# Performance work log

Measured on AMD Instinct MI355X. Metric: run time of the kernel, lower is better.

## Reference

```python
import jax, jax.numpy as jnp
import numpy as np

NUM_EMBED = 512
EMBED_DIM = 64
COMMITMENT_COST = 0.25
DECAY = 0.99
LAPLACE_ALPHA = 1e-05


def setup_inputs() -> dict:
    key = jax.random.key(0)
    k1, k2 = jax.random.split(key, 2)
    inputs = jax.random.normal(k1, (4, EMBED_DIM, 32, 32, 32), dtype=jnp.float32)
    embed = jax.random.normal(k2, (NUM_EMBED, EMBED_DIM), dtype=jnp.float32)
    # buffers: embed_avg starts as a clone of embed; cluster_size at steady state (post first pass)
    embed_avg = embed
    cluster_size = jnp.ones((NUM_EMBED,), dtype=jnp.float32)
    return {"inputs": inputs, "embed": embed, "embed_avg": embed_avg, "cluster_size": cluster_size}


def reference(inputs, embed, embed_avg, cluster_size):
    # channel-last flatten: [B,C,D,H,W] -> [B,D,H,W,C] -> [N,C]
    channel_last = jnp.transpose(inputs, (0, 2, 3, 4, 1))
    input_shape = channel_last.shape
    flat_input = channel_last.reshape(-1, EMBED_DIM)  # [N, C]
    n_tokens = flat_input.shape[0]

    distances = ((flat_input ** 2).sum(axis=1, keepdims=True)
                 + (embed ** 2).sum(axis=1)
                 - 2.0 * flat_input @ embed.T)
    encoding_indices = jnp.argmin(distances, axis=1)  # [N]

    quantized_cl = embed[encoding_indices].reshape(input_shape)  # gather + reshape

    # --- EMA codebook update (training branch), all non-differentiable ---
    # new_cluster_size = one_hot.sum(0); dw = one_hot.T @ flat_input  (as segment sums)
    new_counts = jax.ops.segment_sum(jnp.ones((n_tokens,), flat_input.dtype),
                                     encoding_indices, num_segments=NUM_EMBED)
    dw = jax.ops.segment_sum(flat_input, encoding_indices, num_segments=NUM_EMBED)  # [K, C]
    new_cluster_size = cluster_size * DECAY + (1.0 - DECAY) * new_counts
    new_embed_avg = embed_avg * DECAY + (1.0 - DECAY) * dw
    n = new_cluster_size.sum()
    smoothed = n * ((new_cluster_size + LAPLACE_ALPHA) / (n + NUM_EMBED * LAPLACE_ALPHA))
    new_embed = new_embed_avg / smoothed[:, None]

    # perplexity from empirical code usage
    avg_probs = new_counts / n_tokens
    perplexity = jnp.exp(-jnp.sum(avg_probs * jnp.log(avg_probs + 1e-10)))

    quantized_cf = jnp.transpose(quantized_cl, (0, 4, 1, 2, 3))  # back to [B,C,D,H,W]

    # commitment loss (quantized is detached in original; everything above is no_grad)
    e_latent_loss = jnp.mean((quantized_cf - inputs) ** 2)
    loss = COMMITMENT_COST * e_latent_loss

    # straight-through estimator
    quantized_out = inputs + jax.lax.stop_gradient(quantized_cf - inputs)

    encoding_indices = encoding_indices.reshape(input_shape[:-1])
    return (loss, quantized_out, perplexity, encoding_indices,
            new_embed, new_cluster_size, new_embed_avg)
```

## Files before the change

### kernel.cpp

```cpp
#include <hip/hip_runtime.h>
#include <math.h>

typedef __attribute__((ext_vector_type(8))) short s16x8;
typedef __attribute__((ext_vector_type(4))) float f32x4;

#define B_    4
#define C_    64
#define S_    32768
#define N_    131072
#define K_    512
#define SPLITS 8
#define DECAY_ 0.99f
#define ONEM_  0.01f
#define ALPHA_ 1e-5f
#define DELTA_ 0.01f
#define AMB_CAP 65536

#define OFF_LOSS 0
#define OFF_Q    1
#define OFF_PERP 8388609
#define OFF_IDX  8388610
#define OFF_NEMB 8519682
#define OFF_NCS  8552450
#define OFF_NEA  8552962

#define WS_LOSS   0
#define WS_AMBN   8
#define WS_CNT    16
#define WS_CUR    528
#define WS_OFFS   1040
#define WS_SMOOTH 1552
#define WS_E2     2064
#define WS_SORT   2576
#define WS_PART   133648
#define WS_SPL    395792
#define WS_AMB    444944
#define WS_ET     510480

__device__ __forceinline__ ushort f2bf(float f) {
    uint u = __float_as_uint(f);
    u = u + 0x7FFFu + ((u >> 16) & 1u);
    return (ushort)(u >> 16);
}
__device__ __forceinline__ float bf2f(ushort h) {
    return __uint_as_float(((uint)h) << 16);
}

__global__ __launch_bounds__(256) void k_split(const float* __restrict__ embed,
                                               float* __restrict__ wsf) {
    const int t = threadIdx.x;
    const int lane = t & 63;
    const int code = blockIdx.x * 4 + (t >> 6);
    const float e = embed[code * C_ + lane];
    const float sc = -2.f * e;
    const ushort h1 = f2bf(sc);
    const ushort h2 = f2bf(sc - bf2f(h1));
    ushort* tab = (ushort*)(wsf + WS_SPL);
    tab[0 * (K_ * C_) + code * C_ + lane] = h1;
    tab[1 * (K_ * C_) + code * C_ + lane] = h2;
    wsf[WS_ET + lane * K_ + code] = e;
    float sq = e * e;
    for (int o = 32; o > 0; o >>= 1) sq += __shfl_down(sq, o, 64);
    if (lane == 0) wsf[WS_E2 + code] = sq;
}

__global__ __launch_bounds__(256) void k_assign(const float* __restrict__ in,
                                                float* __restrict__ out,
                                                float* __restrict__ wsf,
                                                int* __restrict__ wsi) {
    __shared__ float s_e2l[K_];
    __shared__ int   s_cnt[K_];
    __shared__ float s_x2[256];
    __shared__ float s_loss;

    const int t = threadIdx.x;
    const int lane = t & 63;
    const int w = t >> 6;
    const int col = lane & 15;
    const int quad = lane >> 4;

    for (int i = t; i < K_; i += 256) { s_e2l[i] = wsf[WS_E2 + i]; s_cnt[i] = 0; }
    if (t == 0) s_loss = 0.f;

    const int nw = blockIdx.x * 256 + w * 64;

    s16x8 a[4][2][2];
#pragma unroll
    for (int j = 0; j < 4; ++j) {
        const int n = nw + j * 16 + col;
        const int base = ((n >> 15) << 21) + (n & (S_ - 1));
        float x0[8], x1[8];
#pragma unroll
        for (int q = 0; q < 8; ++q) {
            x0[q] = in[base + ((quad * 8 + q) << 15)];
            x1[q] = in[base + ((32 + quad * 8 + q) << 15)];
        }
        float x2 = 0.f;
#pragma unroll
        for (int q = 0; q < 8; ++q) x2 += x0[q] * x0[q] + x1[q] * x1[q];
        x2 += __shfl_xor(x2, 16, 64);
        x2 += __shfl_xor(x2, 32, 64);
        if (quad == 0) s_x2[w * 64 + j * 16 + col] = x2;

        float4* q0 = (float4*)(out + OFF_Q + (size_t)n * C_ + quad * 8);
        q0[0] = make_float4(x0[0], x0[1], x0[2], x0[3]);
        q0[1] = make_float4(x0[4], x0[5], x0[6], x0[7]);
        float4* q1 = (float4*)(out + OFF_Q + (size_t)n * C_ + 32 + quad * 8);
        q1[0] = make_float4(x1[0], x1[1], x1[2], x1[3]);
        q1[1] = make_float4(x1[4], x1[5], x1[6], x1[7]);

#pragma unroll
        for (int q = 0; q < 8; ++q) {
            ushort h = f2bf(x0[q]); a[j][0][0][q] = (short)h;
            a[j][1][0][q] = (short)f2bf(x0[q] - bf2f(h));
            h = f2bf(x1[q]); a[j][0][1][q] = (short)h;
            a[j][1][1][q] = (short)f2bf(x1[q] - bf2f(h));
        }
    }
    __syncthreads();

    const s16x8* tab = (const s16x8*)(wsf + WS_SPL);
    float bestd[4][4], bestd2[4][4];
    int   besti[4][4];
#pragma unroll
    for (int j = 0; j < 4; ++j)
#pragma unroll
        for (int r = 0; r < 4; ++r) { bestd[j][r] = 3.4e38f; bestd2[j][r] = 3.4e38f; besti[j][r] = 0; }

    int o = col * 8 + quad;
    s16x8 bh0 = tab[o], bh1 = tab[o + 4];
    s16x8 bl0 = tab[4096 + o], bl1 = tab[4096 + o + 4];

    for (int ct = 0; ct < 32; ++ct) {
        s16x8 nh0, nh1, nl0, nl1;
        if (ct < 31) {
            const int on = o + 128;
            nh0 = tab[on];        nh1 = tab[on + 4];
            nl0 = tab[4096 + on]; nl1 = tab[4096 + on + 4];
        }
        const float e2c = s_e2l[ct * 16 + col];
        f32x4 acc[4];
#pragma unroll
        for (int j = 0; j < 4; ++j) acc[j] = (f32x4){e2c, e2c, e2c, e2c};
#pragma unroll
        for (int j = 0; j < 4; ++j) acc[j] = __builtin_amdgcn_mfma_f32_16x16x32_bf16(a[j][1][0], bh0, acc[j], 0, 0, 0);
#pragma unroll
        for (int j = 0; j < 4; ++j) acc[j] = __builtin_amdgcn_mfma_f32_16x16x32_bf16(a[j][1][1], bh1, acc[j], 0, 0, 0);
#pragma unroll
        for (int j = 0; j < 4; ++j) acc[j] = __builtin_amdgcn_mfma_f32_16x16x32_bf16(a[j][0][0], bl0, acc[j], 0, 0, 0);
#pragma unroll
        for (int j = 0; j < 4; ++j) acc[j] = __builtin_amdgcn_mfma_f32_16x16x32_bf16(a[j][0][1], bl1, acc[j], 0, 0, 0);
#pragma unroll
        for (int j = 0; j < 4; ++j) acc[j] = __builtin_amdgcn_mfma_f32_16x16x32_bf16(a[j][0][0], bh0, acc[j], 0, 0, 0);
#pragma unroll
        for (int j = 0; j < 4; ++j) acc[j] = __builtin_amdgcn_mfma_f32_16x16x32_bf16(a[j][0][1], bh1, acc[j], 0, 0, 0);

        const int code = ct * 16 + col;
#pragma unroll
        for (int j = 0; j < 4; ++j) {
#pragma unroll
            for (int r = 0; r < 4; ++r) {
                const float av = acc[j][r];
                bestd2[j][r] = fminf(bestd2[j][r], fmaxf(av, bestd[j][r]));
                if (av < bestd[j][r]) { bestd[j][r] = av; besti[j][r] = code; }
            }
        }
        bh0 = nh0; bh1 = nh1; bl0 = nl0; bl1 = nl1;
        o += 128;
    }

    float lsum = 0.f;
#pragma unroll
    for (int j = 0; j < 4; ++j) {
#pragma unroll
        for (int r = 0; r < 4; ++r) {
            float d1 = bestd[j][r], d2 = bestd2[j][r]; int i1 = besti[j][r];
            for (int m = 1; m <= 8; m <<= 1) {
                const float d1o = __shfl_xor(d1, m, 64);
                const int   i1o = __shfl_xor(i1, m, 64);
                const float d2o = __shfl_xor(d2, m, 64);
                if (d1o < d1 || (d1o == d1 && i1o < i1)) {
                    d2 = fminf(d1, d2o); d1 = d1o; i1 = i1o;
                } else {
                    d2 = fminf(d2, d1o);
                }
            }
            if (col == 0) {
                const int tok = j * 16 + quad * 4 + r;
                out[OFF_IDX + nw + tok] = (float)i1;
                atomicAdd(&s_cnt[i1], 1);
                lsum += d1 + s_x2[w * 64 + tok];
                if (d2 - d1 < DELTA_) {
                    const int pos = atomicAdd(&wsi[WS_AMBN], 1);
                    if (pos < AMB_CAP) wsi[WS_AMB + pos] = nw + tok;
                }
            }
        }
    }
    if (col == 0) atomicAdd(&s_loss, lsum);
    __syncthreads();
    for (int i = t; i < K_; i += 256) {
        const int v = s_cnt[i];
        if (v) atomicAdd(&wsi[WS_CNT + i], v);
    }
    if (t == 0) atomicAdd(&wsf[WS_LOSS], s_loss);
}

__global__ __launch_bounds__(256) void k_fixup(float* __restrict__ out,
                                               const float* __restrict__ wsf,
                                               int* __restrict__ wsi) {
    __shared__ float sx[4][C_];
    const int t = threadIdx.x;
    const int lane = t & 63;
    const int w = t >> 6;
    const int gw = blockIdx.x * 4 + w;
    const int nw = gridDim.x * 4;
    int cntA = wsi[WS_AMBN];
    if (cntA > AMB_CAP) cntA = AMB_CAP;
    const float* eT = wsf + WS_ET;

    for (int a = gw; a < cntA; a += nw) {
        const int n = wsi[WS_AMB + a];
        const float xv = out[OFF_Q + (size_t)n * C_ + lane];
        sx[w][lane] = xv;
        float x2 = xv * xv;
        for (int m = 1; m <= 32; m <<= 1) x2 += __shfl_xor(x2, m, 64);

        float bd = 3.4e38f; int bi = 0;
#pragma unroll 2
        for (int q = 0; q < 8; ++q) {
            const int k = (q << 6) + lane;
            float d0 = 0.f, d1 = 0.f, d2 = 0.f, d3 = 0.f;
#pragma unroll
            for (int c = 0; c < C_; c += 4) {
                d0 += sx[w][c + 0] * eT[(c + 0) * K_ + k];
                d1 += sx[w][c + 1] * eT[(c + 1) * K_ + k];
                d2 += sx[w][c + 2] * eT[(c + 2) * K_ + k];
                d3 += sx[w][c + 3] * eT[(c + 3) * K_ + k];
            }
            const float dist = x2 + wsf[WS_E2 + k] - 2.f * ((d0 + d1) + (d2 + d3));
            if (dist < bd) { bd = dist; bi = k; }
        }
        for (int m = 1; m <= 32; m <<= 1) {
            const float db = __shfl_xor(bd, m, 64);
            const int   ib = __shfl_xor(bi, m, 64);
            if (db < bd || (db == bd && ib < bi)) { bd = db; bi = ib; }
        }
        if (lane == 0) {
            const int old = (int)out[OFF_IDX + n];
            if (bi != old) {
                out[OFF_IDX + n] = (float)bi;
                atomicAdd(&wsi[WS_CNT + old], -1);
                atomicAdd(&wsi[WS_CNT + bi], 1);
            }
        }
    }
}

__global__ __launch_bounds__(512) void k_stats(const float* __restrict__ cs,
                                               float* __restrict__ out,
                                               float* __restrict__ wsf,
                                               int* __restrict__ wsi) {
    __shared__ float sf[K_];
    __shared__ int   si[K_];
    const int t = threadIdx.x;

    const int cnt = wsi[WS_CNT + t];
    const float ncs = cs[t] * DECAY_ + ONEM_ * (float)cnt;
    out[OFF_NCS + t] = ncs;

    sf[t] = ncs;
    __syncthreads();
    for (int o = 256; o > 0; o >>= 1) {
        if (t < o) sf[t] += sf[t + o];
        __syncthreads();
    }
    const float n = sf[0];
    __syncthreads();

    const float ap = (float)cnt / (float)N_;
    sf[t] = ap * logf(ap + 1e-10f);
    __syncthreads();
    for (int o = 256; o > 0; o >>= 1) {
        if (t < o) sf[t] += sf[t + o];
        __syncthreads();
    }
    if (t == 0) {
        out[OFF_PERP] = expf(-sf[0]);
        out[OFF_LOSS] = 0.25f * wsf[WS_LOSS] / (float)((long long)N_ * C_);
    }

    wsf[WS_SMOOTH + t] = n * (ncs + ALPHA_) / (n + (float)K_ * ALPHA_);

    si[t] = cnt;
    __syncthreads();
    for (int o = 1; o < K_; o <<= 1) {
        int v = (t >= o) ? si[t - o] : 0;
        __syncthreads();
        si[t] += v;
        __syncthreads();
    }
    wsi[WS_OFFS + t] = si[t] - cnt;
}

#define SCT 1024
__global__ __launch_bounds__(256) void k_scatter(const float* __restrict__ out,
                                                 int* __restrict__ wsi) {
    __shared__ int hc[K_];
    __shared__ int lc[K_];
    __shared__ int codes[SCT];
    const int t = threadIdx.x;
    const int base = blockIdx.x * SCT;

    for (int i = t; i < K_; i += 256) { hc[i] = 0; lc[i] = 0; }
    __syncthreads();
#pragma unroll
    for (int j = 0; j < SCT / 256; ++j) {
        const int k = (int)out[OFF_IDX + base + j * 256 + t];
        codes[j * 256 + t] = k;
        atomicAdd(&hc[k], 1);
    }
    __syncthreads();
    for (int i = t; i < K_; i += 256) {
        const int c = hc[i];
        int gbase = 0;
        if (c > 0) gbase = atomicAdd(&wsi[WS_CUR + i], c);
        hc[i] = wsi[WS_OFFS + i] + gbase;
    }
    __syncthreads();
#pragma unroll
    for (int j = 0; j < SCT / 256; ++j) {
        const int k = codes[j * 256 + t];
        const int pos = atomicAdd(&lc[k], 1);
        wsi[WS_SORT + hc[k] + pos] = base + j * 256 + t;
    }
}

__global__ __launch_bounds__(64) void k_dw_split(float* __restrict__ out,
                                                 float* __restrict__ wsf,
                                                 const int* __restrict__ wsi) {
    const int lane = threadIdx.x;
    const int k = blockIdx.x >> 3;
    const int p = blockIdx.x & (SPLITS - 1);
    const int off = wsi[WS_OFFS + k];
    const int cnt = wsi[WS_CNT + k];
    const int chunk = (cnt + SPLITS - 1) >> 3;
    const int j0 = p * chunk;
    const int j1 = min(j0 + chunk, cnt);
    const float* fx = out + OFF_Q;
    const int* sort = wsi + WS_SORT + off;

    float acc = 0.f;
    for (int base = j0; base < j1; base += 64) {
        const int mcnt = min(64, j1 - base);
        int id = 0;
        if (base + lane < j1) id = sort[base + lane];
        int m = 0;
        for (; m + 8 <= mcnt; m += 8) {
            const int t0 = __shfl(id, m + 0, 64);
            const int t1 = __shfl(id, m + 1, 64);
            const int t2 = __shfl(id, m + 2, 64);
            const int t3 = __shfl(id, m + 3, 64);
            const int t4 = __shfl(id, m + 4, 64);
            const int t5 = __shfl(id, m + 5, 64);
            const int t6 = __shfl(id, m + 6, 64);
            const int t7 = __shfl(id, m + 7, 64);
            const float v0 = fx[(size_t)t0 * C_ + lane];
            const float v1 = fx[(size_t)t1 * C_ + lane];
            const float v2 = fx[(size_t)t2 * C_ + lane];
            const float v3 = fx[(size_t)t3 * C_ + lane];
            const float v4 = fx[(size_t)t4 * C_ + lane];
            const float v5 = fx[(size_t)t5 * C_ + lane];
            const float v6 = fx[(size_t)t6 * C_ + lane];
            const float v7 = fx[(size_t)t7 * C_ + lane];
            acc += ((v0 + v1) + (v2 + v3)) + ((v4 + v5) + (v6 + v7));
        }
        for (; m < mcnt; ++m) {
            const int tk = __shfl(id, m, 64);
            acc += fx[(size_t)tk * C_ + lane];
        }
    }
    wsf[WS_PART + (size_t)blockIdx.x * C_ + lane] = acc;
}

__global__ __launch_bounds__(256) void k_ema(const float* __restrict__ embed_avg,
                                             float* __restrict__ out,
                                             const float* __restrict__ wsf) {
    const int i = blockIdx.x * 256 + threadIdx.x;
    const int k = i >> 6;
    const int c = i & 63;
    float dw = 0.f;
#pragma unroll
    for (int p = 0; p < SPLITS; ++p)
        dw += wsf[WS_PART + (size_t)(k * SPLITS + p) * C_ + c];
    const float nea = embed_avg[i] * DECAY_ + ONEM_ * dw;
    out[OFF_NEA + i] = nea;
    out[OFF_NEMB + i] = nea / wsf[WS_SMOOTH + k];
}

__global__ __launch_bounds__(256) void k_quant(const float* __restrict__ embed,
                                               float* __restrict__ out) {
    const int t = threadIdx.x;
    const int n = blockIdx.x * 256 + t;
    const int b = n >> 15;
    const int s = n & (S_ - 1);
    const int base = (b << 21) + s;
    const int k = (int)out[OFF_IDX + n];
    const float4* er = (const float4*)(embed + k * C_);
#pragma unroll
    for (int q = 0; q < 16; ++q) {
        float4 v = er[q];
        out[OFF_Q + base + ((4*q + 0) << 15)] = v.x;
        out[OFF_Q + base + ((4*q + 1) << 15)] = v.y;
        out[OFF_Q + base + ((4*q + 2) << 15)] = v.z;
        out[OFF_Q + base + ((4*q + 3) << 15)] = v.w;
    }
}

extern "C" void kernel_launch(void* const* d_in, const int* in_sizes, int n_in,
                              void* d_out, int out_size, void* d_ws, size_t ws_size,
                              hipStream_t stream) {
    const float* in        = (const float*)d_in[0];
    const float* embed     = (const float*)d_in[1];
    const float* embed_avg = (const float*)d_in[2];
    const float* cs        = (const float*)d_in[3];
    float* out = (float*)d_out;
    float* wsf = (float*)d_ws;
    int*   wsi = (int*)d_ws;

    hipMemsetAsync(d_ws, 0, (WS_CUR + K_) * sizeof(int), stream);

    k_split   <<<K_ / 4, 256, 0, stream>>>(embed, wsf);
    k_assign  <<<N_ / 256, 256, 0, stream>>>(in, out, wsf, wsi);
    k_fixup   <<<256, 256, 0, stream>>>(out, wsf, wsi);
    k_stats   <<<1, K_, 0, stream>>>(cs, out, wsf, wsi);
    k_scatter <<<N_ / SCT, 256, 0, stream>>>(out, wsi);
    k_dw_split<<<K_ * SPLITS, 64, 0, stream>>>(out, wsf, wsi);
    k_ema     <<<K_ * C_ / 256, 256, 0, stream>>>(embed_avg, out, wsf);
    k_quant   <<<N_ / 256, 256, 0, stream>>>(embed, out);
}
```

Before: 210.5 us.

## Split codebook search across wave pairs and merge partial argmins in LDS

Each block now handles 128 tokens instead of 256. Two waves share each 64-token group, and each wave scans half of the 512 codes. The per-half best and second-best distances and indices are written to shared memory and merged by the first wave before the index, count, loss and ambiguity bookkeeping. This doubles the grid and shortens the per-wave MFMA loop, which should give more parallelism and better latency hiding. In exchange both waves load the input and do the bf16 split redundantly, and an extra barrier and LDS merge are added.

```diff
diff --git a/kernel.cpp b/kernel.cpp
--- a/kernel.cpp
+++ b/kernel.cpp
@@ -70,19 +70,24 @@
                                                 int* __restrict__ wsi) {
     __shared__ float s_e2l[K_];
     __shared__ int   s_cnt[K_];
-    __shared__ float s_x2[256];
+    __shared__ float s_x2[128];
+    __shared__ float s_md1[2][2][64];
+    __shared__ float s_md2[2][2][64];
+    __shared__ int   s_mi1[2][2][64];
     __shared__ float s_loss;
 
     const int t = threadIdx.x;
     const int lane = t & 63;
     const int w = t >> 6;
+    const int p = w >> 1;
+    const int h = w & 1;
     const int col = lane & 15;
     const int quad = lane >> 4;
 
     for (int i = t; i < K_; i += 256) { s_e2l[i] = wsf[WS_E2 + i]; s_cnt[i] = 0; }
     if (t == 0) s_loss = 0.f;
 
-    const int nw = blockIdx.x * 256 + w * 64;
+    const int nw = blockIdx.x * 128 + p * 64;
 
     s16x8 a[4][2][2];
 #pragma unroll
@@ -100,21 +105,23 @@
         for (int q = 0; q < 8; ++q) x2 += x0[q] * x0[q] + x1[q] * x1[q];
         x2 += __shfl_xor(x2, 16, 64);
         x2 += __shfl_xor(x2, 32, 64);
-        if (quad == 0) s_x2[w * 64 + j * 16 + col] = x2;
-
-        float4* q0 = (float4*)(out + OFF_Q + (size_t)n * C_ + quad * 8);
-        q0[0] = make_float4(x0[0], x0[1], x0[2], x0[3]);
-        q0[1] = make_float4(x0[4], x0[5], x0[6], x0[7]);
-        float4* q1 = (float4*)(out + OFF_Q + (size_t)n * C_ + 32 + quad * 8);
-        q1[0] = make_float4(x1[0], x1[1], x1[2], x1[3]);
-        q1[1] = make_float4(x1[4], x1[5], x1[6], x1[7]);
+        if (h == 0 && quad == 0) s_x2[p * 64 + j * 16 + col] = x2;
+
+        if (h == 0) {
+            float4* q0 = (float4*)(out + OFF_Q + (size_t)n * C_ + quad * 8);
+            q0[0] = make_float4(x0[0], x0[1], x0[2], x0[3]);
+            q0[1] = make_float4(x0[4], x0[5], x0[6], x0[7]);
+            float4* q1 = (float4*)(out + OFF_Q + (size_t)n * C_ + 32 + quad * 8);
+            q1[0] = make_float4(x1[0], x1[1], x1[2], x1[3]);
+            q1[1] = make_float4(x1[4], x1[5], x1[6], x1[7]);
+        }
 
 #pragma unroll
         for (int q = 0; q < 8; ++q) {
-            ushort h = f2bf(x0[q]); a[j][0][0][q] = (short)h;
-            a[j][1][0][q] = (short)f2bf(x0[q] - bf2f(h));
-            h = f2bf(x1[q]); a[j][0][1][q] = (short)h;
-            a[j][1][1][q] = (short)f2bf(x1[q] - bf2f(h));
+            ushort hh = f2bf(x0[q]); a[j][0][0][q] = (short)hh;
+            a[j][1][0][q] = (short)f2bf(x0[q] - bf2f(hh));
+            hh = f2bf(x1[q]); a[j][0][1][q] = (short)hh;
+            a[j][1][1][q] = (short)f2bf(x1[q] - bf2f(hh));
         }
     }
     __syncthreads();
@@ -127,13 +134,15 @@
 #pragma unroll
         for (int r = 0; r < 4; ++r) { bestd[j][r] = 3.4e38f; bestd2[j][r] = 3.4e38f; besti[j][r] = 0; }
 
-    int o = col * 8 + quad;
+    int o = col * 8 + quad + h * 2048;
     s16x8 bh0 = tab[o], bh1 = tab[o + 4];
     s16x8 bl0 = tab[4096 + o], bl1 = tab[4096 + o + 4];
-
-    for (int ct = 0; ct < 32; ++ct) {
+    const int ct0 = h * 16;
+
+    for (int cc = 0; cc < 16; ++cc) {
+        const int ct = ct0 + cc;
         s16x8 nh0, nh1, nl0, nl1;
-        if (ct < 31) {
+        if (cc < 15) {
             const int on = o + 128;
             nh0 = tab[on];        nh1 = tab[on + 4];
             nl0 = tab[4096 + on]; nl1 = tab[4096 + on + 4];
@@ -169,7 +178,6 @@
         o += 128;
     }
 
-    float lsum = 0.f;
 #pragma unroll
     for (int j = 0; j < 4; ++j) {
 #pragma unroll
@@ -187,17 +195,41 @@
             }
             if (col == 0) {
                 const int tok = j * 16 + quad * 4 + r;
-                out[OFF_IDX + nw + tok] = (float)i1;
-                atomicAdd(&s_cnt[i1], 1);
-                lsum += d1 + s_x2[w * 64 + tok];
-                if (d2 - d1 < DELTA_) {
-                    const int pos = atomicAdd(&wsi[WS_AMBN], 1);
-                    if (pos < AMB_CAP) wsi[WS_AMB + pos] = nw + tok;
+                s_md1[h][p][tok] = d1;
+                s_md2[h][p][tok] = d2;
+                s_mi1[h][p][tok] = i1;
+            }
+        }
+    }
+    __syncthreads();
+
+    if (h == 0) {
+        float lsum = 0.f;
+#pragma unroll
+        for (int j = 0; j < 4; ++j) {
+#pragma unroll
+            for (int r = 0; r < 4; ++r) {
+                if (col == 0) {
+                    const int tok = j * 16 + quad * 4 + r;
+                    const float d1a = s_md1[0][p][tok], d2a = s_md2[0][p][tok];
+                    const float d1b = s_md1[1][p][tok], d2b = s_md2[1][p][tok];
+                    const int   i1a = s_mi1[0][p][tok], i1b = s_mi1[1][p][tok];
+                    float d1; int i1;
+                    if (d1b < d1a) { d1 = d1b; i1 = i1b; }
+                    else           { d1 = d1a; i1 = i1a; }
+                    const float d2 = fminf(fminf(d2a, d2b), fmaxf(d1a, d1b));
+                    out[OFF_IDX + nw + tok] = (float)i1;
+                    atomicAdd(&s_cnt[i1], 1);
+                    lsum += d1 + s_x2[p * 64 + tok];
+                    if (d2 - d1 < DELTA_) {
+                        const int pos = atomicAdd(&wsi[WS_AMBN], 1);
+                        if (pos < AMB_CAP) wsi[WS_AMB + pos] = nw + tok;
+                    }
                 }
             }
         }
-    }
-    if (col == 0) atomicAdd(&s_loss, lsum);
+        if (col == 0) atomicAdd(&s_loss, lsum);
+    }
     __syncthreads();
     for (int i = t; i < K_; i += 256) {
         const int v = s_cnt[i];
@@ -431,7 +463,7 @@
     hipMemsetAsync(d_ws, 0, (WS_CUR + K_) * sizeof(int), stream);
 
     k_split   <<<K_ / 4, 256, 0, stream>>>(embed, wsf);
-    k_assign  <<<N_ / 256, 256, 0, stream>>>(in, out, wsf, wsi);
+    k_assign  <<<N_ / 128, 256, 0, stream>>>(in, out, wsf, wsi);
     k_fixup   <<<256, 256, 0, stream>>>(out, wsf, wsi);
     k_stats   <<<1, K_, 0, stream>>>(cs, out, wsf, wsi);
     k_scatter <<<N_ / SCT, 256, 0, stream>>>(out, wsi);
```

After: 224.9 us. 6.8% more time.

## Fold stats, memset and EMA into neighbouring kernels to cut launches

Applied to the files above, without the earlier changes.

The separate single-block statistics kernel is removed. Each scatter block now computes the exclusive prefix scan of code counts itself, and the cluster-size, perplexity and loss outputs move into a fused EMA+quantize kernel. The workspace memset becomes a zeroing loop inside block 0 of the first kernel, and the EMA and quantize kernels are merged into one launch. This removes several launches and serialized tiny kernels, at the cost of every block redundantly recomputing the scan and the total count.

```diff
diff --git a/kernel.cpp b/kernel.cpp
--- a/kernel.cpp
+++ b/kernel.cpp
@@ -47,10 +47,14 @@
 }
 
 __global__ __launch_bounds__(256) void k_split(const float* __restrict__ embed,
-                                               float* __restrict__ wsf) {
+                                               float* __restrict__ wsf,
+                                               int* __restrict__ wsi) {
     const int t = threadIdx.x;
     const int lane = t & 63;
     const int code = blockIdx.x * 4 + (t >> 6);
+    if (blockIdx.x == 0) {
+        for (int i = t; i < WS_OFFS; i += 256) wsi[i] = 0;
+    }
     const float e = embed[code * C_ + lane];
     const float sc = -2.f * e;
     const ushort h1 = f2bf(sc);
@@ -257,82 +261,57 @@
     }
 }
 
-__global__ __launch_bounds__(512) void k_stats(const float* __restrict__ cs,
-                                               float* __restrict__ out,
-                                               float* __restrict__ wsf,
-                                               int* __restrict__ wsi) {
-    __shared__ float sf[K_];
-    __shared__ int   si[K_];
-    const int t = threadIdx.x;
-
-    const int cnt = wsi[WS_CNT + t];
-    const float ncs = cs[t] * DECAY_ + ONEM_ * (float)cnt;
-    out[OFF_NCS + t] = ncs;
-
-    sf[t] = ncs;
-    __syncthreads();
-    for (int o = 256; o > 0; o >>= 1) {
-        if (t < o) sf[t] += sf[t + o];
-        __syncthreads();
-    }
-    const float n = sf[0];
-    __syncthreads();
-
-    const float ap = (float)cnt / (float)N_;
-    sf[t] = ap * logf(ap + 1e-10f);
-    __syncthreads();
-    for (int o = 256; o > 0; o >>= 1) {
-        if (t < o) sf[t] += sf[t + o];
-        __syncthreads();
-    }
-    if (t == 0) {
-        out[OFF_PERP] = expf(-sf[0]);
-        out[OFF_LOSS] = 0.25f * wsf[WS_LOSS] / (float)((long long)N_ * C_);
-    }
-
-    wsf[WS_SMOOTH + t] = n * (ncs + ALPHA_) / (n + (float)K_ * ALPHA_);
-
-    si[t] = cnt;
-    __syncthreads();
-    for (int o = 1; o < K_; o <<= 1) {
-        int v = (t >= o) ? si[t - o] : 0;
-        __syncthreads();
-        si[t] += v;
-        __syncthreads();
-    }
-    wsi[WS_OFFS + t] = si[t] - cnt;
-}
-
 #define SCT 1024
 __global__ __launch_bounds__(256) void k_scatter(const float* __restrict__ out,
                                                  int* __restrict__ wsi) {
-    __shared__ int hc[K_];
+    __shared__ int sA[K_];
+    __shared__ int sB[K_];
     __shared__ int lc[K_];
     __shared__ int codes[SCT];
     const int t = threadIdx.x;
     const int base = blockIdx.x * SCT;
 
-    for (int i = t; i < K_; i += 256) { hc[i] = 0; lc[i] = 0; }
+    const int c0 = wsi[WS_CNT + t];
+    const int c1 = wsi[WS_CNT + t + 256];
+    sA[t] = c0; sA[t + 256] = c1;
+    __syncthreads();
+    int* sa = sA; int* sb = sB;
+    for (int o = 1; o < K_; o <<= 1) {
+        const int va = sa[t]       + ((t >= o)       ? sa[t - o]       : 0);
+        const int vb = sa[t + 256] + ((t + 256 >= o) ? sa[t + 256 - o] : 0);
+        sb[t] = va; sb[t + 256] = vb;
+        __syncthreads();
+        int* tmp = sa; sa = sb; sb = tmp;
+    }
+    const int offs0 = sa[t] - c0;
+    const int offs1 = sa[t + 256] - c1;
+    if (blockIdx.x == 0) { wsi[WS_OFFS + t] = offs0; wsi[WS_OFFS + t + 256] = offs1; }
+
+    int* hist = sb;
+    hist[t] = 0; hist[t + 256] = 0;
+    lc[t] = 0;  lc[t + 256] = 0;
     __syncthreads();
 #pragma unroll
     for (int j = 0; j < SCT / 256; ++j) {
         const int k = (int)out[OFF_IDX + base + j * 256 + t];
         codes[j * 256 + t] = k;
-        atomicAdd(&hc[k], 1);
-    }
-    __syncthreads();
-    for (int i = t; i < K_; i += 256) {
-        const int c = hc[i];
-        int gbase = 0;
-        if (c > 0) gbase = atomicAdd(&wsi[WS_CUR + i], c);
-        hc[i] = wsi[WS_OFFS + i] + gbase;
-    }
+        atomicAdd(&hist[k], 1);
+    }
+    __syncthreads();
+    const int ha = hist[t];
+    const int hb = hist[t + 256];
+    int ga = 0, gb = 0;
+    if (ha > 0) ga = atomicAdd(&wsi[WS_CUR + t], ha);
+    if (hb > 0) gb = atomicAdd(&wsi[WS_CUR + t + 256], hb);
+    __syncthreads();
+    hist[t] = offs0 + ga;
+    hist[t + 256] = offs1 + gb;
     __syncthreads();
 #pragma unroll
     for (int j = 0; j < SCT / 256; ++j) {
         const int k = codes[j * 256 + t];
         const int pos = atomicAdd(&lc[k], 1);
-        wsi[WS_SORT + hc[k] + pos] = base + j * 256 + t;
+        wsi[WS_SORT + hist[k] + pos] = base + j * 256 + t;
     }
 }
 
@@ -383,37 +362,69 @@
     wsf[WS_PART + (size_t)blockIdx.x * C_ + lane] = acc;
 }
 
-__global__ __launch_bounds__(256) void k_ema(const float* __restrict__ embed_avg,
-                                             float* __restrict__ out,
-                                             const float* __restrict__ wsf) {
-    const int i = blockIdx.x * 256 + threadIdx.x;
-    const int k = i >> 6;
-    const int c = i & 63;
-    float dw = 0.f;
-#pragma unroll
-    for (int p = 0; p < SPLITS; ++p)
-        dw += wsf[WS_PART + (size_t)(k * SPLITS + p) * C_ + c];
-    const float nea = embed_avg[i] * DECAY_ + ONEM_ * dw;
-    out[OFF_NEA + i] = nea;
-    out[OFF_NEMB + i] = nea / wsf[WS_SMOOTH + k];
-}
-
-__global__ __launch_bounds__(256) void k_quant(const float* __restrict__ embed,
-                                               float* __restrict__ out) {
+__global__ __launch_bounds__(256) void k_emaq(const float* __restrict__ embed,
+                                              const float* __restrict__ embed_avg,
+                                              const float* __restrict__ cs,
+                                              float* __restrict__ out,
+                                              const float* __restrict__ wsf,
+                                              const int* __restrict__ wsi) {
+    __shared__ float sn[256];
+    __shared__ float sncs[K_];
     const int t = threadIdx.x;
-    const int n = blockIdx.x * 256 + t;
+    const int bid = blockIdx.x;
+
+    const int c0 = wsi[WS_CNT + t];
+    const int c1 = wsi[WS_CNT + t + 256];
+    const float ncs0 = cs[t] * DECAY_ + ONEM_ * (float)c0;
+    const float ncs1 = cs[t + 256] * DECAY_ + ONEM_ * (float)c1;
+    sncs[t] = ncs0; sncs[t + 256] = ncs1;
+    sn[t] = ncs0 + ncs1;
+    __syncthreads();
+    for (int o = 128; o > 0; o >>= 1) { if (t < o) sn[t] += sn[t + o]; __syncthreads(); }
+    const float ntot = sn[0];
+    __syncthreads();
+
+    if (bid == 0) {
+        out[OFF_NCS + t] = ncs0;
+        out[OFF_NCS + t + 256] = ncs1;
+        const float ap0 = (float)c0 / (float)N_;
+        const float ap1 = (float)c1 / (float)N_;
+        sn[t] = ap0 * logf(ap0 + 1e-10f) + ap1 * logf(ap1 + 1e-10f);
+        __syncthreads();
+        for (int o = 128; o > 0; o >>= 1) { if (t < o) sn[t] += sn[t + o]; __syncthreads(); }
+        if (t == 0) {
+            out[OFF_PERP] = expf(-sn[0]);
+            out[OFF_LOSS] = 0.25f * wsf[WS_LOSS] / (float)((long long)N_ * C_);
+        }
+    }
+
+    if (bid < 128) {
+        const int i = bid * 256 + t;
+        const int k = i >> 6;
+        const int c = i & 63;
+        const float smooth = ntot * (sncs[k] + ALPHA_) / (ntot + (float)K_ * ALPHA_);
+        float dw = 0.f;
+#pragma unroll
+        for (int p = 0; p < SPLITS; ++p)
+            dw += wsf[WS_PART + (size_t)(k * SPLITS + p) * C_ + c];
+        const float nea = embed_avg[i] * DECAY_ + ONEM_ * dw;
+        out[OFF_NEA + i] = nea;
+        out[OFF_NEMB + i] = nea / smooth;
+    }
+
+    const int n = bid * 256 + t;
     const int b = n >> 15;
     const int s = n & (S_ - 1);
-    const int base = (b << 21) + s;
+    const int qbase = (b << 21) + s;
     const int k = (int)out[OFF_IDX + n];
     const float4* er = (const float4*)(embed + k * C_);
 #pragma unroll
     for (int q = 0; q < 16; ++q) {
         float4 v = er[q];
-        out[OFF_Q + base + ((4*q + 0) << 15)] = v.x;
-        out[OFF_Q + base + ((4*q + 1) << 15)] = v.y;
-        out[OFF_Q + base + ((4*q + 2) << 15)] = v.z;
-        out[OFF_Q + base + ((4*q + 3) << 15)] = v.w;
+        out[OFF_Q + qbase + ((4 * q + 0) << 15)] = v.x;
+        out[OFF_Q + qbase + ((4 * q + 1) << 15)] = v.y;
+        out[OFF_Q + qbase + ((4 * q + 2) << 15)] = v.z;
+        out[OFF_Q + qbase + ((4 * q + 3) << 15)] = v.w;
     }
 }
 
@@ -428,14 +439,10 @@
     float* wsf = (float*)d_ws;
     int*   wsi = (int*)d_ws;
 
-    hipMemsetAsync(d_ws, 0, (WS_CUR + K_) * sizeof(int), stream);
-
-    k_split   <<<K_ / 4, 256, 0, stream>>>(embed, wsf);
+    k_split   <<<K_ / 4, 256, 0, stream>>>(embed, wsf, wsi);
     k_assign  <<<N_ / 256, 256, 0, stream>>>(in, out, wsf, wsi);
     k_fixup   <<<256, 256, 0, stream>>>(out, wsf, wsi);
-    k_stats   <<<1, K_, 0, stream>>>(cs, out, wsf, wsi);
     k_scatter <<<N_ / SCT, 256, 0, stream>>>(out, wsi);
     k_dw_split<<<K_ * SPLITS, 64, 0, stream>>>(out, wsf, wsi);
-    k_ema     <<<K_ * C_ / 256, 256, 0, stream>>>(embed_avg, out, wsf);
-    k_quant   <<<N_ / 256, 256, 0, stream>>>(embed, out);
-}
+    k_emaq    <<<N_ / 256, 256, 0, stream>>>(embed, embed_avg, cs, out, wsf, wsi);
+}
```

Result: faster. 203.5 us (-3.3%).
